# Optimization experiments

Measured on AMD Instinct MI355X. Metric: run time of the kernel, lower is better.

## Reference

```python
import jax, jax.numpy as jnp
import numpy as np

B, L, H, NH = 4, 1024, 768, 12      # docs, seq len, hidden, attn heads
E, M, P = 30, 8, 512                # entities/doc, mentions/entity, ht pairs/doc
NLAB = 97                           # DocRED relation count
EMB, BLK = 768, 64                  # emb_size, block_size
OFFSET = 1                          # bert cls offset


def setup_inputs() -> dict:
    key = jax.random.key(0)
    ks = jax.random.split(key, 24)
    def n(k, shp, s=0.02):
        return jax.random.normal(k, shp, jnp.float32) * s
    seq_out = jax.random.normal(ks[0], (B, L, H), jnp.float32)
    attn = jax.random.uniform(ks[1], (B, NH, L, L), jnp.float32)
    mention_idx = jax.random.randint(ks[2], (B, E, M), 0, L - 2)
    ht_pairs = jax.random.randint(ks[3], (B, P, 2), 0, E)
    label_emb = jax.random.normal(ks[4], (NLAB, H), jnp.float32)
    adj = (jax.random.uniform(ks[5], (NLAB, NLAB)) < 0.2).astype(jnp.int32)
    label_adj = jnp.maximum(adj, jnp.eye(NLAB, dtype=jnp.int32))  # self loops
    return dict(
        seq_out=seq_out, attn=attn, mention_idx=mention_idx, ht_pairs=ht_pairs,
        label_adj=label_adj, label_emb=label_emb,
        gW0=n(ks[6], (H, 2 * 500)), gal0=n(ks[7], (2, 500)), gar0=n(ks[8], (2, 500)),
        gW1=n(ks[9], (1000, 2 * 500)), gal1=n(ks[10], (2, 500)), gar1=n(ks[11], (2, 500)),
        gW2=n(ks[12], (1000, H)), gal2=n(ks[13], (1, H)), gar2=n(ks[14], (1, H)),
        ln_gamma=jnp.ones((NLAB,), jnp.float32), ln_beta=jnp.zeros((NLAB,), jnp.float32),
        W_lin2=n(ks[15], (2 * NLAB, NLAB)), b_lin2=jnp.zeros((NLAB,), jnp.float32),
        W_head=n(ks[16], (2 * H, EMB)), b_head=jnp.zeros((EMB,), jnp.float32),
        W_tail=n(ks[17], (2 * H, EMB)), b_tail=jnp.zeros((EMB,), jnp.float32),
        W_bil=n(ks[18], (EMB * BLK + NLAB, NLAB)), b_bil=jnp.zeros((NLAB,), jnp.float32),
    )


def _gat_layer(x, W, al, ar, adj, act):
    nh, od = al.shape
    z = (x @ W).reshape(x.shape[0], nh, od)          # [N, nh, od]
    el = (z * al[None]).sum(-1)                      # src scores [N, nh]
    er = (z * ar[None]).sum(-1)                      # dst scores [N, nh]
    e = jax.nn.leaky_relu(er[:, None, :] + el[None, :, :], 0.2)  # [dst, src, nh]
    e = jnp.where((adj.T > 0)[:, :, None], e, -1e9)
    a = jax.nn.softmax(e, axis=1)
    out = jnp.einsum('vuh,uhd->vhd', a, z)
    return act(out) if act is not None else out


def _layer_norm(x, g, b, eps=1e-5):
    m = x.mean(-1, keepdims=True)
    v = ((x - m) ** 2).mean(-1, keepdims=True)
    return (x - m) * jax.lax.rsqrt(v + eps) * g + b


def _forward(seq_out, attn, label_emb, gW0, gal0, gar0, gW1, gal1, gar1,
             gW2, gal2, gar2, ln_gamma, ln_beta, W_lin2, b_lin2,
             W_head, b_head, W_tail, b_tail, W_bil, b_bil,
             mention_idx, ht_pairs, label_adj):
    pos = mention_idx + OFFSET                                   # [B,E,M]
    bidx3 = jnp.arange(B)[:, None, None]
    ment_emb = seq_out[bidx3, pos]                               # [B,E,M,H]
    ent_emb = jax.nn.logsumexp(ment_emb, axis=2)                 # [B,E,H]
    ment_att = attn[bidx3, :, pos]                               # [B,E,M,NH,L]
    ent_att = ment_att.mean(2)                                   # [B,E,NH,L]

    bidx2 = jnp.arange(B)[:, None]
    h_idx, t_idx = ht_pairs[..., 0], ht_pairs[..., 1]            # [B,P]
    hs = ent_emb[bidx2, h_idx]                                   # [B,P,H]
    ts = ent_emb[bidx2, t_idx]
    ht_att = (ent_att[bidx2, h_idx] * ent_att[bidx2, t_idx]).mean(2)  # [B,P,L]
    ht_att = ht_att / (ht_att.sum(-1, keepdims=True) + 1e-5)
    rs = jnp.einsum('bld,brl->brd', seq_out, ht_att)             # [B,P,H]

    N = B * P
    hs, ts, rs = hs.reshape(N, H), ts.reshape(N, H), rs.reshape(N, H)

    # label GAT: 2 hidden layers (2 heads, concat) + output head
    x = _gat_layer(label_emb, gW0, gal0, gar0, label_adj, None).reshape(NLAB, -1)
    x = jax.nn.elu(x)
    x = _gat_layer(x, gW1, gal1, gar1, label_adj, None).reshape(NLAB, -1)
    x = jax.nn.elu(x)
    lab = _gat_layer(x, gW2, gal2, gar2, label_adj, None).reshape(NLAB, H)

    hs_li = _layer_norm(hs @ lab.T, ln_gamma, ln_beta)           # [N,97]
    ts_li = _layer_norm(ts @ lab.T, ln_gamma, ln_beta)
    logits_li = jnp.concatenate([hs_li, ts_li], axis=1) @ W_lin2 + b_lin2

    hs2 = jnp.tanh(jnp.concatenate([hs, rs], axis=1) @ W_head + b_head)
    ts2 = jnp.tanh(jnp.concatenate([ts, rs], axis=1) @ W_tail + b_tail)
    b1 = hs2.reshape(N, EMB // BLK, BLK)
    b2 = ts2.reshape(N, EMB // BLK, BLK)
    bl = (b1[:, :, :, None] * b2[:, :, None, :]).reshape(N, EMB * BLK)
    logits = jnp.concatenate([bl, logits_li], axis=1) @ W_bil + b_bil
    return logits


def reference(seq_out, attn, mention_idx, ht_pairs, label_adj, label_emb,
              gW0, gal0, gar0, gW1, gal1, gar1, gW2, gal2, gar2,
              ln_gamma, ln_beta, W_lin2, b_lin2, W_head, b_head,
              W_tail, b_tail, W_bil, b_bil):
    return _forward(seq_out, attn, label_emb, gW0, gal0, gar0, gW1, gal1, gar1,
                    gW2, gal2, gar2, ln_gamma, ln_beta, W_lin2, b_lin2,
                    W_head, b_head, W_tail, b_tail, W_bil, b_bil,
                    mention_idx, ht_pairs, label_adj)
```

## Files before the change

kernel.cpp:

```cpp
#include <hip/hip_runtime.h>
#include <hip/hip_bf16.h>
#include <math.h>

typedef __hip_bfloat16 bf16;

__device__ __forceinline__ float toF(float x){ return x; }
__device__ __forceinline__ float toF(bf16 x){ return __bfloat162float(x); }
__device__ __forceinline__ void storeF(float v, float* p){ *p = v; }
__device__ __forceinline__ void storeF(float v, bf16* p){ *p = __float2bfloat16(v); }

__device__ __forceinline__ float bfLo(unsigned u){ return __uint_as_float(u << 16); }
__device__ __forceinline__ float bfHi(unsigned u){ return __uint_as_float(u & 0xFFFF0000u); }

__device__ __forceinline__ bool gateOff(const int* flag, int want){
    return flag && (*flag != want);
}

__global__ void detect_kernel(const unsigned int* gamma_bits, int* flag){
    if (threadIdx.x == 0) *flag = (gamma_bits[0] == 0x3F800000u) ? 0 : 1;
}

template<typename T>
__global__ void cvt_in(const T* __restrict__ in, float* __restrict__ out, int n,
                       const int* flag, int want){
    if (gateOff(flag, want)) return;
    int i = blockIdx.x*256 + threadIdx.x;
    if (i < n) out[i] = toF(in[i]);
}

template<typename T>
__global__ void store_out(const float* __restrict__ in, T* __restrict__ out, int n,
                          const int* flag, int want){
    if (gateOff(flag, want)) return;
    int i = blockIdx.x*256 + threadIdx.x;
    if (i < n) storeF(in[i], &out[i]);
}

template<typename T>
__global__ void ent_emb_kernel(const T* __restrict__ seq, const int* __restrict__ midx,
                               float* __restrict__ ent_emb, const int* flag, int want){
    if (gateOff(flag, want)) return;
    int be = blockIdx.x;
    int b  = be / 30;
    __shared__ int pos[8];
    if (threadIdx.x < 8) pos[threadIdx.x] = midx[be*8 + threadIdx.x] + 1;
    __syncthreads();
    for (int h = threadIdx.x; h < 768; h += 256){
        float v[8], mx = -1e30f;
        #pragma unroll
        for (int m=0;m<8;m++){
            v[m] = toF(seq[((size_t)b*1024 + pos[m])*768 + h]);
            mx = fmaxf(mx, v[m]);
        }
        float s = 0.f;
        #pragma unroll
        for (int m=0;m<8;m++) s += __expf(v[m]-mx);
        ent_emb[(size_t)be*768 + h] = mx + __logf(s);
    }
}

template<typename T>
__global__ void ent_att_kernel(const T* __restrict__ attn, const int* __restrict__ midx,
                               float* __restrict__ ent_att, const int* flag, int want){
    if (gateOff(flag, want)) return;
    int id = blockIdx.x;
    int nh = id % 12, be = id / 12, b = be / 30;
    __shared__ int pos[8];
    if (threadIdx.x < 8) pos[threadIdx.x] = midx[be*8 + threadIdx.x] + 1;
    __syncthreads();
    const size_t base = ((size_t)(b*12 + nh))*1024*1024;
    for (int l = threadIdx.x; l < 1024; l += 256){
        float s = 0.f;
        #pragma unroll
        for (int m=0;m<8;m++) s += toF(attn[base + (size_t)pos[m]*1024 + l]);
        ent_att[((size_t)be*12 + nh)*1024 + l] = s * 0.125f;
    }
}

__global__ void pair_kernel(const float* __restrict__ ent_emb, const float* __restrict__ ent_att,
                            const int* __restrict__ htp,
                            float* __restrict__ hs, float* __restrict__ ts, float* __restrict__ ht_att){
    int n = blockIdx.x;
    int b = n >> 9;
    int h = htp[n*2], t = htp[n*2+1];
    const float* eh = ent_emb + ((size_t)b*30 + h)*768;
    const float* et = ent_emb + ((size_t)b*30 + t)*768;
    for (int d = threadIdx.x; d < 768; d += 256){
        hs[(size_t)n*768 + d] = eh[d];
        ts[(size_t)n*768 + d] = et[d];
    }
    const float* ah = ent_att + ((size_t)b*30 + h)*12*1024;
    const float* at = ent_att + ((size_t)b*30 + t)*12*1024;
    float loc[4]; float psum = 0.f;
    #pragma unroll
    for (int i=0;i<4;i++){
        int l = threadIdx.x + i*256;
        float s = 0.f;
        #pragma unroll
        for (int k=0;k<12;k++) s += ah[k*1024 + l]*at[k*1024 + l];
        s *= (1.f/12.f);
        loc[i] = s; psum += s;
    }
    __shared__ float red[256];
    red[threadIdx.x] = psum; __syncthreads();
    for (int off=128; off>0; off>>=1){
        if (threadIdx.x < off) red[threadIdx.x] += red[threadIdx.x+off];
        __syncthreads();
    }
    float inv = 1.f/(red[0] + 1e-5f);
    #pragma unroll
    for (int i=0;i<4;i++){
        int l = threadIdx.x + i*256;
        ht_att[(size_t)n*1024 + l] = loc[i]*inv;
    }
}

template<typename T>
__global__ void rs_kernel(const T* __restrict__ seq, const float* __restrict__ ht_att,
                          float* __restrict__ rs, const int* flag, int want){
    if (gateOff(flag, want)) return;
    int hc = blockIdx.x;
    int pt = blockIdx.y;
    int b  = blockIdx.z;
    int h  = hc*256 + threadIdx.x;
    float acc[16];
    #pragma unroll
    for (int i=0;i<16;i++) acc[i]=0.f;
    __shared__ __align__(16) float att[64][20];
    for (int l0=0; l0<1024; l0+=64){
        for (int idx=threadIdx.x; idx<1024; idx+=256){
            int pl = idx>>6, lo = idx&63;
            att[lo][pl] = ht_att[((size_t)(b*512 + pt*16 + pl))*1024 + l0 + lo];
        }
        __syncthreads();
        for (int lo=0; lo<64; lo++){
            float sv = toF(seq[((size_t)b*1024 + l0 + lo)*768 + h]);
            #pragma unroll
            for (int p=0;p<16;p++) acc[p] += att[lo][p]*sv;
        }
        __syncthreads();
    }
    #pragma unroll
    for (int p=0;p<16;p++)
        rs[((size_t)(b*512 + pt*16 + p))*768 + h] = acc[p];
}

template<typename TB>
__global__ __launch_bounds__(256) void gemm64(const float* __restrict__ A1, const float* __restrict__ A2,
                                              int K1, int K, const TB* __restrict__ B,
                                              const TB* __restrict__ bias, int act,
                                              float* __restrict__ C, int M, int N,
                                              const int* flag, int want){
    if (gateOff(flag, want)) return;
    __shared__ __align__(16) float As[32][68];
    __shared__ __align__(16) float Bs[32][68];
    int m0 = blockIdx.y*64, n0 = blockIdx.x*64;
    int tid = threadIdx.x;
    int tr = tid>>4, tc = tid&15;
    float acc[4][4];
    #pragma unroll
    for (int i=0;i<4;i++)
        #pragma unroll
        for (int j=0;j<4;j++) acc[i][j]=0.f;
    int K2 = K - K1;
    for (int k0=0; k0<K; k0+=32){
        for (int e=tid; e<2048; e+=256){
            int k=e&31, m=e>>5;
            int gm=m0+m, gk=k0+k;
            float v=0.f;
            if (gm<M && gk<K) v = (gk<K1)? A1[(size_t)gm*K1+gk] : A2[(size_t)gm*K2 + (gk-K1)];
            As[k][m]=v;
        }
        for (int e=tid; e<2048; e+=256){
            int nn=e&63, k=e>>6;
            int gk=k0+k, gn=n0+nn;
            float v=0.f;
            if (gk<K && gn<N) v = toF(B[(size_t)gk*N+gn]);
            Bs[k][nn]=v;
        }
        __syncthreads();
        #pragma unroll
        for (int kk=0;kk<32;kk++){
            float4 a4 = *(const float4*)&As[kk][tr<<2];
            float4 b4 = *(const float4*)&Bs[kk][tc<<2];
            float av[4]={a4.x,a4.y,a4.z,a4.w}, bv[4]={b4.x,b4.y,b4.z,b4.w};
            #pragma unroll
            for (int i=0;i<4;i++)
                #pragma unroll
                for (int j=0;j<4;j++) acc[i][j] += av[i]*bv[j];
        }
        __syncthreads();
    }
    #pragma unroll
    for (int i=0;i<4;i++){
        int m = m0 + (tr<<2) + i;
        if (m >= M) continue;
        #pragma unroll
        for (int j=0;j<4;j++){
            int n = n0 + (tc<<2) + j;
            if (n >= N) continue;
            float v = acc[i][j];
            if (bias) v += toF(bias[n]);
            if (act == 1) v = tanhf(v);
            C[(size_t)m*N + n] = v;
        }
    }
}

template<typename T>
__global__ void elr_kernel(const float* __restrict__ z, const T* __restrict__ al,
                           const T* __restrict__ ar, int nh, int od,
                           float* __restrict__ el, float* __restrict__ er,
                           const int* flag, int want){
    if (gateOff(flag, want)) return;
    int u = blockIdx.x;
    __shared__ float sl[256], sr[256];
    int tid = threadIdx.x;
    for (int h=0; h<nh; h++){
        float a=0.f, r=0.f;
        for (int d=tid; d<od; d+=256){
            float zz = z[((size_t)u*nh + h)*od + d];
            a += zz*toF(al[h*od+d]);
            r += zz*toF(ar[h*od+d]);
        }
        sl[tid]=a; sr[tid]=r; __syncthreads();
        for (int off=128; off>0; off>>=1){
            if (tid<off){ sl[tid]+=sl[tid+off]; sr[tid]+=sr[tid+off]; }
            __syncthreads();
        }
        if (tid==0){ el[u*nh+h]=sl[0]; er[u*nh+h]=sr[0]; }
        __syncthreads();
    }
}

__global__ void gat_agg_kernel(const float* __restrict__ z, const float* __restrict__ el,
                               const float* __restrict__ er, const int* __restrict__ adj,
                               int nh, int od, int applyElu, float* __restrict__ out){
    int v = blockIdx.x;
    int tid = threadIdx.x;
    __shared__ float e[2][97];
    int D = nh*od;
    for (int idx=tid; idx<97*nh; idx+=256){
        int u = idx % 97, h = idx / 97;
        float ev;
        if (adj[u*97 + v] > 0){
            ev = er[v*nh+h] + el[u*nh+h];
            ev = ev > 0.f ? ev : 0.2f*ev;
        } else ev = -1e9f;
        e[h][u] = ev;
    }
    __syncthreads();
    if (tid < nh){
        float mx=-1e30f;
        for (int u2=0;u2<97;u2++) mx = fmaxf(mx, e[tid][u2]);
        float s=0.f;
        for (int u2=0;u2<97;u2++){ float x=__expf(e[tid][u2]-mx); e[tid][u2]=x; s+=x; }
        float inv = 1.f/s;
        for (int u2=0;u2<97;u2++) e[tid][u2]*=inv;
    }
    __syncthreads();
    for (int d0=tid; d0<D; d0+=256){
        int h = d0 / od;
        float s = 0.f;
        for (int u2=0;u2<97;u2++) s += e[h][u2]*z[(size_t)u2*D + d0];
        if (applyElu) s = s>0.f ? s : expm1f(s);
        out[(size_t)v*D + d0] = s;
    }
}

__global__ void transpose_kernel(const float* __restrict__ lab, float* __restrict__ labT){
    int i = blockIdx.x*256 + threadIdx.x;
    if (i < 97*768){ int c = i/768, k = i%768; labT[(size_t)k*97 + c] = lab[i]; }
}

template<typename T>
__global__ void ln_kernel(const float* __restrict__ in, const T* __restrict__ gamma,
                          const T* __restrict__ beta, float* __restrict__ out,
                          const int* flag, int want){
    if (gateOff(flag, want)) return;
    int n = blockIdx.x;
    int tid = threadIdx.x;
    __shared__ float red[128];
    float v = (tid < 97) ? in[(size_t)n*97 + tid] : 0.f;
    red[tid] = v; __syncthreads();
    for (int off=64; off>0; off>>=1){
        if (tid<off) red[tid]+=red[tid+off];
        __syncthreads();
    }
    float mean = red[0]*(1.f/97.f); __syncthreads();
    float d = (tid < 97) ? v - mean : 0.f;
    red[tid] = d*d; __syncthreads();
    for (int off=64; off>0; off>>=1){
        if (tid<off) red[tid]+=red[tid+off];
        __syncthreads();
    }
    float rstd = rsqrtf(red[0]*(1.f/97.f) + 1e-5f);
    if (tid < 97)
        out[(size_t)n*97 + tid] = d*rstd*toF(gamma[tid]) + toF(beta[tid]);
}

template<typename T>
__global__ __launch_bounds__(256) void bilinear_kernel(const float* __restrict__ hs2,
                                                       const float* __restrict__ ts2,
                                                       const T* __restrict__ Wb,
                                                       float* __restrict__ out,
                                                       const int* flag, int want){
    if (gateOff(flag, want)) return;
    int nb = blockIdx.x, g = blockIdx.y, ih = blockIdx.z;
    int n0 = nb*32;
    __shared__ __align__(16) float hsb[16][36];
    __shared__ __align__(16) float tsb[64][36];
    __shared__ __align__(16) float wbuf[2][3104];
    int tid = threadIdx.x;
    for (int e=tid; e<512; e+=256){
        int i = e&15, nl = e>>4;
        hsb[i][nl] = hs2[(size_t)(n0+nl)*768 + g*64 + ih*16 + i];
    }
    for (int e=tid; e<2048; e+=256){
        int j = e&63, nl = e>>6;
        tsb[j][nl] = ts2[(size_t)(n0+nl)*768 + g*64 + j];
    }
    const T* Wg = Wb + (size_t)g*4096*97 + (size_t)ih*16*6208;

    if constexpr (sizeof(T) == 4){
        const float4* src = (const float4*)Wg;
        float4* dst = (float4*)wbuf[0];
        #pragma unroll
        for (int u=0;u<4;u++){ int e = tid + u*256; if (e < 776) dst[e] = src[e]; }
    } else {
        const uint4* src = (const uint4*)Wg;
        #pragma unroll
        for (int u=0;u<2;u++){
            int e = tid + u*256;
            if (e < 388){
                uint4 w = src[e];
                float* d = &wbuf[0][e*8];
                d[0]=bfLo(w.x); d[1]=bfHi(w.x); d[2]=bfLo(w.y); d[3]=bfHi(w.y);
                d[4]=bfLo(w.z); d[5]=bfHi(w.z); d[6]=bfLo(w.w); d[7]=bfHi(w.w);
            }
        }
    }
    __syncthreads();

    int cg = tid & 63;
    int ng = tid >> 6;
    int c0 = cg, c1 = cg + 64;
    bool c1ok = (c1 < 97);
    float acc0[8], acc1[8];
    #pragma unroll
    for (int q=0;q<8;q++){ acc0[q]=0.f; acc1[q]=0.f; }

    int cur = 0;
    for (int k=0; k<32; ++k){
        int i = k>>1;
        float4 wreg[4];
        uint4  breg[2];
        if (k+1 < 32){
            if constexpr (sizeof(T) == 4){
                const float4* src = (const float4*)(Wg + (size_t)(k+1)*3104);
                #pragma unroll
                for (int u=0;u<4;u++){ int e = tid + u*256; if (e < 776) wreg[u] = src[e]; }
            } else {
                const uint4* src = (const uint4*)(Wg + (size_t)(k+1)*3104);
                #pragma unroll
                for (int u=0;u<2;u++){ int e = tid + u*256; if (e < 388) breg[u] = src[e]; }
            }
        }
        float a[8];
        #pragma unroll
        for (int q=0;q<8;q++) a[q] = hsb[i][ng*8+q];
        float s0[8], s1[8];
        #pragma unroll
        for (int q=0;q<8;q++){ s0[q]=0.f; s1[q]=0.f; }
        const float* wrow = wbuf[cur];
        int jbase = (k&1)*32;
        #pragma unroll 2
        for (int j=0;j<32;j++){
            float w0 = wrow[j*97 + c0];
            float w1 = c1ok ? wrow[j*97 + c1] : 0.f;
            const float4* tp = (const float4*)&tsb[jbase + j][ng*8];
            float4 t0 = tp[0], t1 = tp[1];
            float tv[8] = {t0.x,t0.y,t0.z,t0.w,t1.x,t1.y,t1.z,t1.w};
            #pragma unroll
            for (int q=0;q<8;q++){ s0[q] += tv[q]*w0; s1[q] += tv[q]*w1; }
        }
        #pragma unroll
        for (int q=0;q<8;q++){ acc0[q] += a[q]*s0[q]; acc1[q] += a[q]*s1[q]; }
        if (k+1 < 32){
            if constexpr (sizeof(T) == 4){
                float4* dst = (float4*)wbuf[cur^1];
                #pragma unroll
                for (int u=0;u<4;u++){ int e = tid + u*256; if (e < 776) dst[e] = wreg[u]; }
            } else {
                float* base = wbuf[cur^1];
                #pragma unroll
                for (int u=0;u<2;u++){
                    int e = tid + u*256;
                    if (e < 388){
                        uint4 w = breg[u];
                        float* d = &base[e*8];
                        d[0]=bfLo(w.x); d[1]=bfHi(w.x); d[2]=bfLo(w.y); d[3]=bfHi(w.y);
                        d[4]=bfLo(w.z); d[5]=bfHi(w.z); d[6]=bfLo(w.w); d[7]=bfHi(w.w);
                    }
                }
            }
        }
        __syncthreads();
        cur ^= 1;
    }
    #pragma unroll
    for (int q=0;q<8;q++){
        int n = n0 + ng*8 + q;
        atomicAdd(&out[(size_t)n*97 + c0], acc0[q]);
        if (c1ok) atomicAdd(&out[(size_t)n*97 + c1], acc1[q]);
    }
}

extern "C" void kernel_launch(void* const* d_in, const int* in_sizes, int n_in,
                              void* d_out, int out_size, void* d_ws, size_t ws_size,
                              hipStream_t stream){
    (void)in_sizes; (void)n_in; (void)ws_size; (void)out_size;
    const void* seq   = d_in[0];
    const void* attn  = d_in[1];
    const int*  midx  = (const int*)d_in[2];
    const int*  htp   = (const int*)d_in[3];
    const int*  adj   = (const int*)d_in[4];
    const void* lemb  = d_in[5];
    const void* gW0   = d_in[6];
    const void* gal0  = d_in[7];
    const void* gar0  = d_in[8];
    const void* gW1   = d_in[9];
    const void* gal1  = d_in[10];
    const void* gar1  = d_in[11];
    const void* gW2   = d_in[12];
    const void* gal2  = d_in[13];
    const void* gar2  = d_in[14];
    const void* ln_g  = d_in[15];
    const void* ln_b  = d_in[16];
    const void* Wlin2 = d_in[17];
    const void* blin2 = d_in[18];
    const void* Whead = d_in[19];
    const void* bhead = d_in[20];
    const void* Wtail = d_in[21];
    const void* btail = d_in[22];
    const void* Wbil  = d_in[23];
    const void* bbil  = d_in[24];

    int*   flag = (int*)d_ws;
    float* base = (float*)d_ws + 16;
    float* hs     = base;
    float* ts     = hs + 1572864;
    float* R2     = ts + 1572864;
    float* ht_att = R2;
    float* hs2    = R2;
    float* li_raw = R2 + 1572864;
    float* R3     = R2 + 2097152;
    float* ent_emb= R3;
    float* ent_att= R3 + 92160;
    float* li     = R3;
    float* ts2    = R3;
    float* rs     = R3 + 1572864;
    float* sm     = rs + 1572864;
    float* x0   = sm;
    float* zbuf = x0 + 74496;
    float* x1   = zbuf + 97000;
    float* x2   = x1 + 97000;
    float* lab  = x2 + 97000;
    float* labT = lab + 74496;
    float* el   = labT + 74496;
    float* er   = el + 194;
    float* ll   = er + 194;
    float* logits = ll + 198656;

    detect_kernel<<<1,64,0,stream>>>((const unsigned int*)ln_g, flag);

    ent_emb_kernel<float><<<120,256,0,stream>>>((const float*)seq, midx, ent_emb, flag, 0);
    ent_emb_kernel<bf16 ><<<120,256,0,stream>>>((const bf16* )seq, midx, ent_emb, flag, 1);
    ent_att_kernel<float><<<1440,256,0,stream>>>((const float*)attn, midx, ent_att, flag, 0);
    ent_att_kernel<bf16 ><<<1440,256,0,stream>>>((const bf16* )attn, midx, ent_att, flag, 1);
    pair_kernel<<<2048,256,0,stream>>>(ent_emb, ent_att, htp, hs, ts, ht_att);
    rs_kernel<float><<<dim3(3,32,4),256,0,stream>>>((const float*)seq, ht_att, rs, flag, 0);
    rs_kernel<bf16 ><<<dim3(3,32,4),256,0,stream>>>((const bf16* )seq, ht_att, rs, flag, 1);

    cvt_in<float><<<(74496+255)/256,256,0,stream>>>((const float*)lemb, x0, 74496, flag, 0);
    cvt_in<bf16 ><<<(74496+255)/256,256,0,stream>>>((const bf16* )lemb, x0, 74496, flag, 1);

    auto gemm_pair = [&](const float* A1, const float* A2, int K1, int K,
                         const void* B, const void* bias, int act,
                         float* C, int M, int N, dim3 grid){
        gemm64<float><<<grid,256,0,stream>>>(A1,A2,K1,K,(const float*)B,(const float*)bias,act,C,M,N,flag,0);
        gemm64<bf16 ><<<grid,256,0,stream>>>(A1,A2,K1,K,(const bf16* )B,(const bf16* )bias,act,C,M,N,flag,1);
    };
    auto elr_pair = [&](const float* z, const void* al, const void* ar, int nh, int od){
        elr_kernel<float><<<97,256,0,stream>>>(z,(const float*)al,(const float*)ar,nh,od,el,er,flag,0);
        elr_kernel<bf16 ><<<97,256,0,stream>>>(z,(const bf16* )al,(const bf16* )ar,nh,od,el,er,flag,1);
    };

    gemm_pair(x0, nullptr, 768, 768, gW0, nullptr, 0, zbuf, 97, 1000, dim3(16,2));
    elr_pair(zbuf, gal0, gar0, 2, 500);
    gat_agg_kernel<<<97,256,0,stream>>>(zbuf, el, er, adj, 2, 500, 1, x1);
    gemm_pair(x1, nullptr, 1000, 1000, gW1, nullptr, 0, zbuf, 97, 1000, dim3(16,2));
    elr_pair(zbuf, gal1, gar1, 2, 500);
    gat_agg_kernel<<<97,256,0,stream>>>(zbuf, el, er, adj, 2, 500, 1, x2);
    gemm_pair(x2, nullptr, 1000, 1000, gW2, nullptr, 0, zbuf, 97, 768, dim3(12,2));
    elr_pair(zbuf, gal2, gar2, 1, 768);
    gat_agg_kernel<<<97,256,0,stream>>>(zbuf, el, er, adj, 1, 768, 0, lab);
    transpose_kernel<<<(74496+255)/256,256,0,stream>>>(lab, labT);

    gemm64<float><<<dim3(2,64),256,0,stream>>>(hs, nullptr, 768, 768, labT,
        (const float*)nullptr, 0, li_raw, 4096, 97, nullptr, 0);
    ln_kernel<float><<<4096,128,0,stream>>>(li_raw, (const float*)ln_g, (const float*)ln_b, li, flag, 0);
    ln_kernel<bf16 ><<<4096,128,0,stream>>>(li_raw, (const bf16* )ln_g, (const bf16* )ln_b, li, flag, 1);
    gemm_pair(li, li + 2048*97, 97, 194, Wlin2, blin2, 0, ll, 2048, 97, dim3(2,32));

    gemm_pair(hs, rs, 768, 1536, Whead, bhead, 1, hs2, 2048, 768, dim3(12,32));
    gemm_pair(ts, rs, 768, 1536, Wtail, btail, 1, ts2, 2048, 768, dim3(12,32));

    gemm64<float><<<dim3(2,32),256,0,stream>>>(ll, nullptr, 97, 97,
        (const float*)Wbil + (size_t)49152*97, (const float*)bbil, 0, logits, 2048, 97, flag, 0);
    gemm64<bf16 ><<<dim3(2,32),256,0,stream>>>(ll, nullptr, 97, 97,
        (const bf16* )Wbil + (size_t)49152*97, (const bf16* )bbil, 0, logits, 2048, 97, flag, 1);

    bilinear_kernel<float><<<dim3(64,12,4),256,0,stream>>>(hs2, ts2, (const float*)Wbil, logits, flag, 0);
    bilinear_kernel<bf16 ><<<dim3(64,12,4),256,0,stream>>>(hs2, ts2, (const bf16* )Wbil, logits, flag, 1);

    store_out<float><<<(198656+255)/256,256,0,stream>>>(logits, (float*)d_out, 198656, flag, 0);
    store_out<bf16 ><<<(198656+255)/256,256,0,stream>>>(logits, (bf16*)d_out, 198656, flag, 1);
}
```

Before: 2.623 ms.

## Reorder bilinear weight staging to reuse ts values across head rows

Changes the bilinear kernel's loop order. Each staged weight chunk now covers 8 head-block rows by 4 tail columns instead of 1 row by 32 columns. Tail values for 4 j-indices are kept in registers and reused across 8 i-rows, which cuts shared-memory reads of tsb. The trade-off is strided, less coalesced global weight loads with per-thread div/mod index math, and more registers held live.

```diff
diff --git a/kernel.cpp b/kernel.cpp
--- a/kernel.cpp
+++ b/kernel.cpp
@@ -320,23 +320,33 @@
         int j = e&63, nl = e>>6;
         tsb[j][nl] = ts2[(size_t)(n0+nl)*768 + g*64 + j];
     }
-    const T* Wg = Wb + (size_t)g*4096*97 + (size_t)ih*16*6208;
+    int il4[4], pp4[4];
+    #pragma unroll
+    for (int u=0;u<4;u++){
+        int e = tid + u*256;
+        il4[u] = e/97;
+        pp4[u] = e - il4[u]*97;
+    }
+    const size_t base_u = (size_t)g*99328 + (size_t)ih*24832;
 
     if constexpr (sizeof(T) == 4){
-        const float4* src = (const float4*)Wg;
+        const float4* src = (const float4*)Wb + base_u;
         float4* dst = (float4*)wbuf[0];
         #pragma unroll
-        for (int u=0;u<4;u++){ int e = tid + u*256; if (e < 776) dst[e] = src[e]; }
+        for (int u=0;u<4;u++){
+            int e = tid + u*256;
+            if (e < 776) dst[e] = src[(size_t)il4[u]*1552 + pp4[u]];
+        }
     } else {
-        const uint4* src = (const uint4*)Wg;
-        #pragma unroll
-        for (int u=0;u<2;u++){
+        const uint2* src = (const uint2*)Wb + base_u;
+        float4* dst = (float4*)wbuf[0];
+        #pragma unroll
+        for (int u=0;u<4;u++){
             int e = tid + u*256;
-            if (e < 388){
-                uint4 w = src[e];
-                float* d = &wbuf[0][e*8];
-                d[0]=bfLo(w.x); d[1]=bfHi(w.x); d[2]=bfLo(w.y); d[3]=bfHi(w.y);
-                d[4]=bfLo(w.z); d[5]=bfHi(w.z); d[6]=bfLo(w.w); d[7]=bfHi(w.w);
+            if (e < 776){
+                uint2 w = src[(size_t)il4[u]*1552 + pp4[u]];
+                float4 d; d.x=bfLo(w.x); d.y=bfHi(w.x); d.z=bfLo(w.y); d.w=bfHi(w.y);
+                dst[e] = d;
             }
         }
     }
@@ -351,62 +361,86 @@
     for (int q=0;q<8;q++){ acc0[q]=0.f; acc1[q]=0.f; }
 
     int cur = 0;
-    for (int k=0; k<32; ++k){
-        int i = k>>1;
-        float4 wreg[4];
-        uint4  breg[2];
-        if (k+1 < 32){
-            if constexpr (sizeof(T) == 4){
-                const float4* src = (const float4*)(Wg + (size_t)(k+1)*3104);
-                #pragma unroll
-                for (int u=0;u<4;u++){ int e = tid + u*256; if (e < 776) wreg[u] = src[e]; }
-            } else {
-                const uint4* src = (const uint4*)(Wg + (size_t)(k+1)*3104);
-                #pragma unroll
-                for (int u=0;u<2;u++){ int e = tid + u*256; if (e < 388) breg[u] = src[e]; }
-            }
-        }
-        float a[8];
-        #pragma unroll
-        for (int q=0;q<8;q++) a[q] = hsb[i][ng*8+q];
-        float s0[8], s1[8];
-        #pragma unroll
-        for (int q=0;q<8;q++){ s0[q]=0.f; s1[q]=0.f; }
-        const float* wrow = wbuf[cur];
-        int jbase = (k&1)*32;
-        #pragma unroll 2
-        for (int j=0;j<32;j++){
-            float w0 = wrow[j*97 + c0];
-            float w1 = c1ok ? wrow[j*97 + c1] : 0.f;
-            const float4* tp = (const float4*)&tsb[jbase + j][ng*8];
+    for (int jq=0; jq<16; ++jq){
+        float tv[4][8];
+        #pragma unroll
+        for (int jj=0;jj<4;jj++){
+            const float4* tp = (const float4*)&tsb[jq*4+jj][ng*8];
             float4 t0 = tp[0], t1 = tp[1];
-            float tv[8] = {t0.x,t0.y,t0.z,t0.w,t1.x,t1.y,t1.z,t1.w};
-            #pragma unroll
-            for (int q=0;q<8;q++){ s0[q] += tv[q]*w0; s1[q] += tv[q]*w1; }
-        }
-        #pragma unroll
-        for (int q=0;q<8;q++){ acc0[q] += a[q]*s0[q]; acc1[q] += a[q]*s1[q]; }
-        if (k+1 < 32){
-            if constexpr (sizeof(T) == 4){
-                float4* dst = (float4*)wbuf[cur^1];
-                #pragma unroll
-                for (int u=0;u<4;u++){ int e = tid + u*256; if (e < 776) dst[e] = wreg[u]; }
-            } else {
-                float* base = wbuf[cur^1];
-                #pragma unroll
-                for (int u=0;u<2;u++){
-                    int e = tid + u*256;
-                    if (e < 388){
-                        uint4 w = breg[u];
-                        float* d = &base[e*8];
-                        d[0]=bfLo(w.x); d[1]=bfHi(w.x); d[2]=bfLo(w.y); d[3]=bfHi(w.y);
-                        d[4]=bfLo(w.z); d[5]=bfHi(w.z); d[6]=bfLo(w.w); d[7]=bfHi(w.w);
+            tv[jj][0]=t0.x; tv[jj][1]=t0.y; tv[jj][2]=t0.z; tv[jj][3]=t0.w;
+            tv[jj][4]=t1.x; tv[jj][5]=t1.y; tv[jj][6]=t1.z; tv[jj][7]=t1.w;
+        }
+        for (int h2=0; h2<2; ++h2){
+            int nxt = jq*2 + h2 + 1;
+            float4 wreg[4];
+            uint2  breg[4];
+            if (nxt < 32){
+                int jqn = nxt>>1, h2n = nxt&1;
+                size_t off = base_u + (size_t)h2n*12416 + (size_t)jqn*97;
+                if constexpr (sizeof(T) == 4){
+                    const float4* src = (const float4*)Wb + off;
+                    #pragma unroll
+                    for (int u=0;u<4;u++){
+                        int e = tid + u*256;
+                        if (e < 776) wreg[u] = src[(size_t)il4[u]*1552 + pp4[u]];
+                    }
+                } else {
+                    const uint2* src = (const uint2*)Wb + off;
+                    #pragma unroll
+                    for (int u=0;u<4;u++){
+                        int e = tid + u*256;
+                        if (e < 776) breg[u] = src[(size_t)il4[u]*1552 + pp4[u]];
                     }
                 }
             }
-        }
-        __syncthreads();
-        cur ^= 1;
+            const float* wch = wbuf[cur];
+            #pragma unroll 2
+            for (int il=0; il<8; ++il){
+                int i = h2*8 + il;
+                const float4* ap = (const float4*)&hsb[i][ng*8];
+                float4 a0 = ap[0], a1 = ap[1];
+                float a[8] = {a0.x,a0.y,a0.z,a0.w,a1.x,a1.y,a1.z,a1.w};
+                const float* w0p = wch + il*388;
+                float s0[8], s1[8];
+                {
+                    float w0 = w0p[c0];
+                    float w1 = c1ok ? w0p[c1] : 0.f;
+                    #pragma unroll
+                    for (int q=0;q<8;q++){ s0[q] = tv[0][q]*w0; s1[q] = tv[0][q]*w1; }
+                }
+                #pragma unroll
+                for (int jj=1;jj<4;jj++){
+                    float w0 = w0p[jj*97 + c0];
+                    float w1 = c1ok ? w0p[jj*97 + c1] : 0.f;
+                    #pragma unroll
+                    for (int q=0;q<8;q++){ s0[q] += tv[jj][q]*w0; s1[q] += tv[jj][q]*w1; }
+                }
+                #pragma unroll
+                for (int q=0;q<8;q++){ acc0[q] += a[q]*s0[q]; acc1[q] += a[q]*s1[q]; }
+            }
+            if (nxt < 32){
+                float4* dstb = (float4*)wbuf[cur^1];
+                if constexpr (sizeof(T) == 4){
+                    #pragma unroll
+                    for (int u=0;u<4;u++){
+                        int e = tid + u*256;
+                        if (e < 776) dstb[e] = wreg[u];
+                    }
+                } else {
+                    #pragma unroll
+                    for (int u=0;u<4;u++){
+                        int e = tid + u*256;
+                        if (e < 776){
+                            uint2 w = breg[u];
+                            float4 d; d.x=bfLo(w.x); d.y=bfHi(w.x); d.z=bfLo(w.y); d.w=bfHi(w.y);
+                            dstb[e] = d;
+                        }
+                    }
+                }
+            }
+            __syncthreads();
+            cur ^= 1;
+        }
     }
     #pragma unroll
     for (int q=0;q<8;q++){
```

Measured after the change: 2.663 ms. No clear change (+1.5%).

## Compute per-entity projections before gathering pairs instead of per-pair GEMMs

Applied to the files above, without the earlier changes.

Since hs/ts are gathered entity embeddings, the head/tail projections of the entity part, the label-interaction GEMM, layer norm and lin2 halves are computed once per entity (120 rows) instead of per pair (2048 rows). Per-pair results are then obtained by gathering and adding, with tanh applied in a separate elementwise kernel after the rs-only GEMM. This removes the hs/ts materialization and roughly halves the K of the large head/tail GEMMs, at the cost of extra small kernels and an extra read-modify-write pass over hs2/ts2.

```diff
diff --git a/kernel.cpp b/kernel.cpp
--- a/kernel.cpp
+++ b/kernel.cpp
@@ -77,18 +77,12 @@
     }
 }
 
-__global__ void pair_kernel(const float* __restrict__ ent_emb, const float* __restrict__ ent_att,
+__global__ void pair_kernel(const float* __restrict__ ent_att,
                             const int* __restrict__ htp,
-                            float* __restrict__ hs, float* __restrict__ ts, float* __restrict__ ht_att){
+                            float* __restrict__ ht_att){
     int n = blockIdx.x;
     int b = n >> 9;
     int h = htp[n*2], t = htp[n*2+1];
-    const float* eh = ent_emb + ((size_t)b*30 + h)*768;
-    const float* et = ent_emb + ((size_t)b*30 + t)*768;
-    for (int d = threadIdx.x; d < 768; d += 256){
-        hs[(size_t)n*768 + d] = eh[d];
-        ts[(size_t)n*768 + d] = et[d];
-    }
     const float* ah = ent_att + ((size_t)b*30 + h)*12*1024;
     const float* at = ent_att + ((size_t)b*30 + t)*12*1024;
     float loc[4]; float psum = 0.f;
@@ -297,6 +291,30 @@
     float rstd = rsqrtf(red[0]*(1.f/97.f) + 1e-5f);
     if (tid < 97)
         out[(size_t)n*97 + tid] = d*rstd*toF(gamma[tid]) + toF(beta[tid]);
+}
+
+template<typename T>
+__global__ void ll_kernel(const float* __restrict__ Eh2, const float* __restrict__ Et2,
+                          const int* __restrict__ htp, const T* __restrict__ blin2,
+                          float* __restrict__ ll, const int* flag, int want){
+    if (gateOff(flag, want)) return;
+    int n = blockIdx.x;
+    int b = n >> 9;
+    int h = htp[n*2], t = htp[n*2+1];
+    int c = threadIdx.x;
+    if (c < 97)
+        ll[(size_t)n*97 + c] = Eh2[(size_t)(b*30+h)*97 + c]
+                             + Et2[(size_t)(b*30+t)*97 + c] + toF(blin2[c]);
+}
+
+__global__ void addtanh_kernel(float* __restrict__ X, const float* __restrict__ EW,
+                               const int* __restrict__ htp, int sel){
+    int d = blockIdx.x*256 + threadIdx.x;
+    int n = blockIdx.y;
+    int b = n >> 9;
+    int e = htp[n*2 + sel];
+    size_t xi = (size_t)n*768 + d;
+    X[xi] = tanhf(X[xi] + EW[(size_t)(b*30+e)*768 + d]);
 }
 
 template<typename T>
@@ -448,19 +466,21 @@
 
     int*   flag = (int*)d_ws;
     float* base = (float*)d_ws + 16;
-    float* hs     = base;
-    float* ts     = hs + 1572864;
-    float* R2     = ts + 1572864;
+    float* EWh  = base;
+    float* EWt  = EWh + 92160;
+    float* EL   = EWt + 92160;
+    float* ELn  = EL  + 11640;
+    float* Eh2  = ELn + 11640;
+    float* Et2  = Eh2 + 11640;
+    float* R2     = base + 2*1572864;
     float* ht_att = R2;
     float* hs2    = R2;
-    float* li_raw = R2 + 1572864;
     float* R3     = R2 + 2097152;
     float* ent_emb= R3;
     float* ent_att= R3 + 92160;
-    float* li     = R3;
     float* ts2    = R3;
     float* rs     = R3 + 1572864;
-    float* sm     = rs + 1572864;
+    float* sm   = rs + 1572864;
     float* x0   = sm;
     float* zbuf = x0 + 74496;
     float* x1   = zbuf + 97000;
@@ -478,12 +498,9 @@
     ent_emb_kernel<bf16 ><<<120,256,0,stream>>>((const bf16* )seq, midx, ent_emb, flag, 1);
     ent_att_kernel<float><<<1440,256,0,stream>>>((const float*)attn, midx, ent_att, flag, 0);
     ent_att_kernel<bf16 ><<<1440,256,0,stream>>>((const bf16* )attn, midx, ent_att, flag, 1);
-    pair_kernel<<<2048,256,0,stream>>>(ent_emb, ent_att, htp, hs, ts, ht_att);
+    pair_kernel<<<2048,256,0,stream>>>(ent_att, htp, ht_att);
     rs_kernel<float><<<dim3(3,32,4),256,0,stream>>>((const float*)seq, ht_att, rs, flag, 0);
     rs_kernel<bf16 ><<<dim3(3,32,4),256,0,stream>>>((const bf16* )seq, ht_att, rs, flag, 1);
-
-    cvt_in<float><<<(74496+255)/256,256,0,stream>>>((const float*)lemb, x0, 74496, flag, 0);
-    cvt_in<bf16 ><<<(74496+255)/256,256,0,stream>>>((const bf16* )lemb, x0, 74496, flag, 1);
 
     auto gemm_pair = [&](const float* A1, const float* A2, int K1, int K,
                          const void* B, const void* bias, int act,
@@ -496,6 +513,12 @@
         elr_kernel<bf16 ><<<97,256,0,stream>>>(z,(const bf16* )al,(const bf16* )ar,nh,od,el,er,flag,1);
     };
 
+    gemm_pair(ent_emb, nullptr, 768, 768, Whead, bhead, 0, EWh, 120, 768, dim3(12,2));
+    gemm_pair(ent_emb, nullptr, 768, 768, Wtail, btail, 0, EWt, 120, 768, dim3(12,2));
+
+    cvt_in<float><<<(74496+255)/256,256,0,stream>>>((const float*)lemb, x0, 74496, flag, 0);
+    cvt_in<bf16 ><<<(74496+255)/256,256,0,stream>>>((const bf16* )lemb, x0, 74496, flag, 1);
+
     gemm_pair(x0, nullptr, 768, 768, gW0, nullptr, 0, zbuf, 97, 1000, dim3(16,2));
     elr_pair(zbuf, gal0, gar0, 2, 500);
     gat_agg_kernel<<<97,256,0,stream>>>(zbuf, el, er, adj, 2, 500, 1, x1);
@@ -507,14 +530,31 @@
     gat_agg_kernel<<<97,256,0,stream>>>(zbuf, el, er, adj, 1, 768, 0, lab);
     transpose_kernel<<<(74496+255)/256,256,0,stream>>>(lab, labT);
 
-    gemm64<float><<<dim3(2,64),256,0,stream>>>(hs, nullptr, 768, 768, labT,
-        (const float*)nullptr, 0, li_raw, 4096, 97, nullptr, 0);
-    ln_kernel<float><<<4096,128,0,stream>>>(li_raw, (const float*)ln_g, (const float*)ln_b, li, flag, 0);
-    ln_kernel<bf16 ><<<4096,128,0,stream>>>(li_raw, (const bf16* )ln_g, (const bf16* )ln_b, li, flag, 1);
-    gemm_pair(li, li + 2048*97, 97, 194, Wlin2, blin2, 0, ll, 2048, 97, dim3(2,32));
-
-    gemm_pair(hs, rs, 768, 1536, Whead, bhead, 1, hs2, 2048, 768, dim3(12,32));
-    gemm_pair(ts, rs, 768, 1536, Wtail, btail, 1, ts2, 2048, 768, dim3(12,32));
+    gemm64<float><<<dim3(2,2),256,0,stream>>>(ent_emb, nullptr, 768, 768, labT,
+        (const float*)nullptr, 0, EL, 120, 97, nullptr, 0);
+    ln_kernel<float><<<120,128,0,stream>>>(EL, (const float*)ln_g, (const float*)ln_b, ELn, flag, 0);
+    ln_kernel<bf16 ><<<120,128,0,stream>>>(EL, (const bf16* )ln_g, (const bf16* )ln_b, ELn, flag, 1);
+    gemm64<float><<<dim3(2,2),256,0,stream>>>(ELn, nullptr, 97, 97,
+        (const float*)Wlin2, (const float*)nullptr, 0, Eh2, 120, 97, flag, 0);
+    gemm64<bf16 ><<<dim3(2,2),256,0,stream>>>(ELn, nullptr, 97, 97,
+        (const bf16* )Wlin2, (const bf16* )nullptr, 0, Eh2, 120, 97, flag, 1);
+    gemm64<float><<<dim3(2,2),256,0,stream>>>(ELn, nullptr, 97, 97,
+        (const float*)Wlin2 + 9409, (const float*)nullptr, 0, Et2, 120, 97, flag, 0);
+    gemm64<bf16 ><<<dim3(2,2),256,0,stream>>>(ELn, nullptr, 97, 97,
+        (const bf16* )Wlin2 + 9409, (const bf16* )nullptr, 0, Et2, 120, 97, flag, 1);
+    ll_kernel<float><<<2048,128,0,stream>>>(Eh2, Et2, htp, (const float*)blin2, ll, flag, 0);
+    ll_kernel<bf16 ><<<2048,128,0,stream>>>(Eh2, Et2, htp, (const bf16* )blin2, ll, flag, 1);
+
+    gemm64<float><<<dim3(12,32),256,0,stream>>>(rs, nullptr, 768, 768,
+        (const float*)Whead + 589824, (const float*)nullptr, 0, hs2, 2048, 768, flag, 0);
+    gemm64<bf16 ><<<dim3(12,32),256,0,stream>>>(rs, nullptr, 768, 768,
+        (const bf16* )Whead + 589824, (const bf16* )nullptr, 0, hs2, 2048, 768, flag, 1);
+    addtanh_kernel<<<dim3(3,2048),256,0,stream>>>(hs2, EWh, htp, 0);
+    gemm64<float><<<dim3(12,32),256,0,stream>>>(rs, nullptr, 768, 768,
+        (const float*)Wtail + 589824, (const float*)nullptr, 0, ts2, 2048, 768, flag, 0);
+    gemm64<bf16 ><<<dim3(12,32),256,0,stream>>>(rs, nullptr, 768, 768,
+        (const bf16* )Wtail + 589824, (const bf16* )nullptr, 0, ts2, 2048, 768, flag, 1);
+    addtanh_kernel<<<dim3(3,2048),256,0,stream>>>(ts2, EWt, htp, 1);
 
     gemm64<float><<<dim3(2,32),256,0,stream>>>(ll, nullptr, 97, 97,
         (const float*)Wbil + (size_t)49152*97, (const float*)bbil, 0, logits, 2048, 97, flag, 0);
```

Result: no change. 2.658 ms (+1.3%).
